# Optimization experiments

Measured on AMD Instinct MI355X. Metric: run time of the kernel, lower is better.

The kernel has to match this reference:

```python
import jax, jax.numpy as jnp
import numpy as np

N_DIM = 128
M_SEQ = 2048
BATCH = 256


def setup_inputs() -> dict:
    key = jax.random.key(0)
    k1, k2, k3 = jax.random.split(key, 3)
    scale = 1.0 / np.sqrt(N_DIM)
    return {
        "x": jax.random.normal(k1, (BATCH, N_DIM, M_SEQ), dtype=jnp.float32),
        "W": jax.random.normal(k2, (N_DIM, 3 * N_DIM), dtype=jnp.float32) * scale,
        "U": jax.random.normal(k3, (N_DIM, 3 * N_DIM), dtype=jnp.float32) * scale,
        "b": jnp.zeros((3 * N_DIM,), dtype=jnp.float32),
    }


def reference(x, W, U, b):
    # x: [B, D, T] -> scan over T with a GRU cell, output [B, D, T]
    B, D, T = x.shape
    xs = jnp.transpose(x, (2, 0, 1))  # [T, B, D]

    def cell(h, xt):
        gx = xt @ W + b              # [B, 3D]
        gh = h @ U                   # [B, 3D]
        xz, xr, xn = jnp.split(gx, 3, axis=-1)
        hz, hr, hn = jnp.split(gh, 3, axis=-1)
        z = jax.nn.sigmoid(xz + hz)  # update gate
        r = jax.nn.sigmoid(xr + hr)  # reset gate
        n = jnp.tanh(xn + r * hn)    # candidate
        h_new = z * h + (1.0 - z) * n
        return h_new, h_new

    h0 = jnp.zeros((B, D), dtype=x.dtype)
    _, ys = jax.lax.scan(cell, h0, xs)   # ys: [T, B, D]
    return jnp.transpose(ys, (1, 2, 0))  # [B, D, T]
```

## Files before the change

kernel.cpp:

```cpp
#include <hip/hip_runtime.h>

typedef float f32x4 __attribute__((ext_vector_type(4)));
typedef short bf16x8 __attribute__((ext_vector_type(8)));

#define TT    2048
#define DDIM  128
#define G3    384
#define NBBLK 16
#define GXROW 6144
#define GX_BYTES ((size_t)NBBLK * TT * GXROW * 2)

__device__ __forceinline__ unsigned f2bf_u(float f) {
    unsigned u = __float_as_uint(f);
    return (u + 0x7FFFu + ((u >> 16) & 1u)) >> 16;
}
__device__ __forceinline__ float bf_lo(unsigned u) { return __uint_as_float(u << 16); }
__device__ __forceinline__ float bf_hi(unsigned u) { return __uint_as_float(u & 0xffff0000u); }
__device__ __forceinline__ float rcp_(float x) { return __builtin_amdgcn_rcpf(x); }
__device__ __forceinline__ float sigm_(float v) { return rcp_(1.0f + __expf(-v)); }
__device__ __forceinline__ float tanhf_(float v) { return 2.0f * rcp_(1.0f + __expf(-2.0f * v)) - 1.0f; }

__global__ __launch_bounds__(256) void gx_gemm(
    const float* __restrict__ x, const float* __restrict__ W,
    const float* __restrict__ bias, unsigned short* __restrict__ gx)
{
    const int bblk  = blockIdx.x;
    const int ttile = blockIdx.y;
    const int tid = threadIdx.x;
    const int w  = tid >> 6;
    const int l  = tid & 63;
    const int lc = l & 15;
    const int lk = l >> 4;

    __shared__ unsigned short xs[16 * 16 * DDIM];

    const int tiles[6] = {2*w, 2*w+1, 2*w+8, 2*w+9, 2*w+16, 2*w+17};

    bf16x8 wfrag[6][4];
    f32x4  binit[6];
    #pragma unroll
    for (int i6 = 0; i6 < 6; ++i6) {
        const int c = tiles[i6] * 16 + lc;
        const float bv = bias[c];
        binit[i6] = (f32x4){bv, bv, bv, bv};
        #pragma unroll
        for (int kt = 0; kt < 4; ++kt) {
            bf16x8 f;
            #pragma unroll
            for (int jj = 0; jj < 8; ++jj) {
                const int k = kt * 32 + lk * 8 + jj;
                f[jj] = (short)f2bf_u(W[k * G3 + c]);
            }
            wfrag[i6][kt] = f;
        }
    }

    int inoff[4];
    #pragma unroll
    for (int kt = 0; kt < 4; ++kt)
        inoff[kt] = (lc * 256 + kt * 64 + lk * 16) ^ ((lc & 7) << 4);

    const float* xb = x + (size_t)bblk * 16 * DDIM * TT;
    const int t0blk = ttile * 128;
    const int tq = tid & 3;
    const int pbase = tid >> 2;

    for (int chunk = 0; chunk < 8; ++chunk) {
        __syncthreads();
        const int t0 = t0blk + chunk * 16 + tq * 4;
        #pragma unroll 4
        for (int pp = 0; pp < 32; ++pp) {
            const int p = pbase + pp * 64;
            const int r = p >> 7, d = p & 127;
            f32x4 v = *(const f32x4*)(xb + (size_t)p * TT + t0);
            const int base = ((r * 128 + d) * 2) ^ ((r & 7) << 4);
            #pragma unroll
            for (int j = 0; j < 4; ++j) {
                const int tloc = tq * 4 + j;
                xs[(tloc * 4096 + base) >> 1] = (unsigned short)f2bf_u(v[j]);
            }
        }
        __syncthreads();

        for (int t = 0; t < 16; ++t) {
            bf16x8 a[4];
            #pragma unroll
            for (int kt = 0; kt < 4; ++kt)
                a[kt] = *(const bf16x8*)((const char*)xs + t * 4096 + inoff[kt]);

            const int tglob = t0blk + chunk * 16 + t;
            #pragma unroll
            for (int i6 = 0; i6 < 6; ++i6) {
                f32x4 acc = binit[i6];
                #pragma unroll
                for (int kt = 0; kt < 4; ++kt)
                    acc = __builtin_amdgcn_mfma_f32_16x16x32_bf16(a[kt], wfrag[i6][kt], acc, 0, 0, 0);
                unsigned p0 = f2bf_u(acc[0]) | (f2bf_u(acc[1]) << 16);
                unsigned p1 = f2bf_u(acc[2]) | (f2bf_u(acc[3]) << 16);
                const int tt6 = tiles[i6];
                const int cb = tt6 & 7, g = tt6 >> 3;
                const size_t off = ((size_t)(bblk * TT + tglob) * 8 + cb) * 768
                                   + g * 256 + l * 4;
                *(uint2*)(gx + off) = make_uint2(p0, p1);
            }
        }
    }
}

__global__ __launch_bounds__(512, 2) void gru_rec(
    const unsigned short* __restrict__ gx, const float* __restrict__ U,
    float* __restrict__ out)
{
    const int bblk = blockIdx.x;
    const int tid  = threadIdx.x;
    const int w  = tid >> 6;
    const int l  = tid & 63;
    const int lc = l & 15, lk = l >> 4;
    const int c  = w * 16 + lc;

    bf16x8 uz[4], ur[4], un[4];
    #pragma unroll
    for (int kt = 0; kt < 4; ++kt) {
        bf16x8 fz, fr, fn;
        #pragma unroll
        for (int jj = 0; jj < 8; ++jj) {
            const int k = kt * 32 + lk * 8 + jj;
            fz[jj] = (short)f2bf_u(U[k * G3 + c]);
            fr[jj] = (short)f2bf_u(U[k * G3 + 128 + c]);
            fn[jj] = (short)f2bf_u(U[k * G3 + 256 + c]);
        }
        uz[kt] = fz; ur[kt] = fr; un[kt] = fn;
    }

    __shared__ unsigned short hsA[2 * 2048];
    __shared__ float hlds[16 * 16 * 128];
    #pragma unroll
    for (int i = tid; i < 4096; i += 512) hsA[i] = 0;

    int roff[4];
    #pragma unroll
    for (int kt = 0; kt < 4; ++kt)
        roff[kt] = (lc * 256 + kt * 64 + lk * 16) ^ ((lc & 7) << 4);

    int widx[4];
    int hwi[4];
    #pragma unroll
    for (int i = 0; i < 4; ++i) {
        const int r = lk * 4 + i;
        widx[i] = (r * 128 + c) ^ ((r & 7) << 3);
        hwi[i]  = r * 128 + (c ^ ((r & 7) << 2));
    }

    float hold[4] = {0.f, 0.f, 0.f, 0.f};

    const unsigned short* g0 = gx + ((size_t)bblk * TT * 8 + w) * 768 + l * 4;

    const int cfl = w * 16 + (l >> 2);
    const int qfl = l & 3;
    float* outfl = out + ((size_t)(bblk * 16) * DDIM + cfl) * TT + qfl * 4;

    uint2 rgz[4], rgr[4], rgn[4];
    #pragma unroll
    for (int d = 0; d < 4; ++d) {
        const unsigned short* gq = g0 + (size_t)d * GXROW;
        rgz[d] = *(const uint2*)(gq);
        rgr[d] = *(const uint2*)(gq + 256);
        rgn[d] = *(const uint2*)(gq + 512);
    }

    __syncthreads();

#define GATE(I, J)                                                            \
    {                                                                         \
        const float zz = sigm_(az[I]);                                        \
        const float rr = sigm_(ar[I]);                                        \
        const float uu = gn##I + rr * an[I];                                  \
        const float nn = tanhf_(uu);                                          \
        const float hn = nn + zz * (hold[I] - nn);                            \
        hold[I] = hn;                                                         \
        hlds[(J) * 2048 + hwi[I]] = hn;                                       \
        hsA[(((J) & 1) ^ 1) * 2048 + widx[I]] = (unsigned short)f2bf_u(hn);   \
    }

#define SUBSTEP(J, DOPF)                                                      \
    {                                                                         \
        uint2 pz = rgz[(J) & 3], pr = rgr[(J) & 3], pn = rgn[(J) & 3];        \
        f32x4 az, ar;                                                         \
        az[0] = bf_lo(pz.x); az[1] = bf_hi(pz.x);                             \
        az[2] = bf_lo(pz.y); az[3] = bf_hi(pz.y);                             \
        ar[0] = bf_lo(pr.x); ar[1] = bf_hi(pr.x);                             \
        ar[2] = bf_lo(pr.y); ar[3] = bf_hi(pr.y);                             \
        const float gn0 = bf_lo(pn.x), gn1 = bf_hi(pn.x);                     \
        const float gn2 = bf_lo(pn.y), gn3 = bf_hi(pn.y);                     \
        if (DOPF) {                                                           \
            const unsigned short* gq = gpt + (size_t)((J) + 4) * GXROW;       \
            rgz[(J) & 3] = *(const uint2*)(gq);                               \
            rgr[(J) & 3] = *(const uint2*)(gq + 256);                         \
            rgn[(J) & 3] = *(const uint2*)(gq + 512);                         \
        }                                                                     \
        const char* hb = (const char*)hsA + ((J) & 1) * 4096;                 \
        bf16x8 a0 = *(const bf16x8*)(hb + roff[0]);                           \
        bf16x8 a1 = *(const bf16x8*)(hb + roff[1]);                           \
        bf16x8 a2 = *(const bf16x8*)(hb + roff[2]);                           \
        bf16x8 a3 = *(const bf16x8*)(hb + roff[3]);                           \
        f32x4 an = (f32x4){0.f, 0.f, 0.f, 0.f};                               \
        az = __builtin_amdgcn_mfma_f32_16x16x32_bf16(a0, uz[0], az, 0, 0, 0); \
        ar = __builtin_amdgcn_mfma_f32_16x16x32_bf16(a0, ur[0], ar, 0, 0, 0); \
        an = __builtin_amdgcn_mfma_f32_16x16x32_bf16(a0, un[0], an, 0, 0, 0); \
        az = __builtin_amdgcn_mfma_f32_16x16x32_bf16(a1, uz[1], az, 0, 0, 0); \
        ar = __builtin_amdgcn_mfma_f32_16x16x32_bf16(a1, ur[1], ar, 0, 0, 0); \
        an = __builtin_amdgcn_mfma_f32_16x16x32_bf16(a1, un[1], an, 0, 0, 0); \
        az = __builtin_amdgcn_mfma_f32_16x16x32_bf16(a2, uz[2], az, 0, 0, 0); \
        ar = __builtin_amdgcn_mfma_f32_16x16x32_bf16(a2, ur[2], ar, 0, 0, 0); \
        an = __builtin_amdgcn_mfma_f32_16x16x32_bf16(a2, un[2], an, 0, 0, 0); \
        az = __builtin_amdgcn_mfma_f32_16x16x32_bf16(a3, uz[3], az, 0, 0, 0); \
        ar = __builtin_amdgcn_mfma_f32_16x16x32_bf16(a3, ur[3], ar, 0, 0, 0); \
        an = __builtin_amdgcn_mfma_f32_16x16x32_bf16(a3, un[3], an, 0, 0, 0); \
        GATE(0, J) GATE(1, J) GATE(2, J) GATE(3, J)                           \
        asm volatile("s_waitcnt lgkmcnt(0)" ::: "memory");                    \
        __builtin_amdgcn_s_barrier();                                         \
    }

#define FLUSH(T0)                                                             \
    _Pragma("unroll")                                                         \
    for (int r = 0; r < 16; ++r) {                                            \
        const int fr = r * 128 + (cfl ^ ((r & 7) << 2));                      \
        f32x4 v;                                                              \
        v[0] = hlds[(qfl * 4 + 0) * 2048 + fr];                               \
        v[1] = hlds[(qfl * 4 + 1) * 2048 + fr];                               \
        v[2] = hlds[(qfl * 4 + 2) * 2048 + fr];                               \
        v[3] = hlds[(qfl * 4 + 3) * 2048 + fr];                               \
        *(f32x4*)(outfl + (size_t)r * (DDIM * TT) + (T0)) = v;                \
    }

    for (int t = 0; t < TT - 16; t += 16) {
        const unsigned short* gpt = g0 + (size_t)t * GXROW;
        SUBSTEP(0, true)  SUBSTEP(1, true)  SUBSTEP(2, true)  SUBSTEP(3, true)
        SUBSTEP(4, true)  SUBSTEP(5, true)  SUBSTEP(6, true)  SUBSTEP(7, true)
        SUBSTEP(8, true)  SUBSTEP(9, true)  SUBSTEP(10, true) SUBSTEP(11, true)
        SUBSTEP(12, true) SUBSTEP(13, true) SUBSTEP(14, true) SUBSTEP(15, true)
        FLUSH(t)
    }
    {
        const int t = TT - 16;
        const unsigned short* gpt = g0 + (size_t)t * GXROW;
        SUBSTEP(0, true)  SUBSTEP(1, true)  SUBSTEP(2, true)  SUBSTEP(3, true)
        SUBSTEP(4, true)  SUBSTEP(5, true)  SUBSTEP(6, true)  SUBSTEP(7, true)
        SUBSTEP(8, true)  SUBSTEP(9, true)  SUBSTEP(10, true) SUBSTEP(11, true)
        SUBSTEP(12, false) SUBSTEP(13, false) SUBSTEP(14, false) SUBSTEP(15, false)
        FLUSH(t)
    }
#undef GATE
#undef SUBSTEP
#undef FLUSH
}

typedef float f32x2 __attribute__((ext_vector_type(2)));

__global__ __launch_bounds__(768) void gru_fused(
    const float* __restrict__ x, const float* __restrict__ W,
    const float* __restrict__ U, const float* __restrict__ b,
    float* __restrict__ out)
{
    const int bb  = blockIdx.x;
    const int tid = threadIdx.x;
    const int kh  = (tid >= G3) ? 1 : 0;
    const int c   = tid - kh * G3;
    const int kbase = kh * 64;

    f32x2 wcol[32], ucol[32];
    #pragma unroll
    for (int k2 = 0; k2 < 32; ++k2) {
        wcol[k2][0] = W[(size_t)(kbase + 2*k2 + 0) * G3 + c];
        wcol[k2][1] = W[(size_t)(kbase + 2*k2 + 1) * G3 + c];
        ucol[k2][0] = U[(size_t)(kbase + 2*k2 + 0) * G3 + c];
        ucol[k2][1] = U[(size_t)(kbase + 2*k2 + 1) * G3 + c];
    }
    const float bias = b[c];

    __shared__ float xs[2][DDIM];
    __shared__ float hs[DDIM];
    __shared__ float px[G3], ph[G3];
    __shared__ float rs[DDIM], ns[DDIM];

    if (tid < DDIM) { hs[tid] = 0.0f; xs[0][tid] = x[((size_t)bb * DDIM + tid) * TT]; }
    __syncthreads();

    const float* __restrict__ xrow = x   + (size_t)bb * DDIM * TT;
    float* __restrict__       orow = out + (size_t)bb * DDIM * TT;
    float zv = 0.0f;

    for (int t = 0; t < TT; ++t) {
        const float* xcur = xs[t & 1] + kbase;
        const float* hcur = hs + kbase;
        f32x2 axv = {0.f, 0.f}, ahv = {0.f, 0.f};
        #pragma unroll
        for (int k2 = 0; k2 < 32; ++k2) {
            f32x2 xv = *(const f32x2*)(xcur + 2*k2);
            f32x2 hv = *(const f32x2*)(hcur + 2*k2);
            axv += xv * wcol[k2];
            ahv += hv * ucol[k2];
        }
        float ax = axv[0] + axv[1];
        float ah = ahv[0] + ahv[1];
        if (kh) { px[c] = ax; ph[c] = ah; }
        if (t + 1 < TT && tid >= 128 && tid < 256) {
            const int k = tid - 128;
            xs[(t + 1) & 1][k] = xrow[(size_t)k * TT + (t + 1)];
        }
        __syncthreads();
        if (!kh) {
            ax += px[c]; ah += ph[c];
            if (c < DDIM)            zv = sigm_(ax + ah + bias);
            else if (c < 2*DDIM)     rs[c - DDIM] = sigm_(ax + ah + bias);
            else { px[c] = ax + bias; ph[c] = ah; }
        }
        __syncthreads();
        if (!kh && c >= 2*DDIM) {
            float r = rs[c - 2*DDIM];
            ns[c - 2*DDIM] = tanhf_(px[c] + r * ph[c]);
        }
        __syncthreads();
        if (tid < DDIM) {
            float n = ns[tid];
            float hnew = zv * hs[tid] + (1.0f - zv) * n;
            hs[tid] = hnew;
            orow[(size_t)tid * TT + t] = hnew;
        }
        __syncthreads();
    }
}

extern "C" void kernel_launch(void* const* d_in, const int* in_sizes, int n_in,
                              void* d_out, int out_size, void* d_ws, size_t ws_size,
                              hipStream_t stream) {
    const float* x = (const float*)d_in[0];
    const float* W = (const float*)d_in[1];
    const float* U = (const float*)d_in[2];
    const float* b = (const float*)d_in[3];
    float* out     = (float*)d_out;

    if (ws_size >= GX_BYTES) {
        unsigned short* gx = (unsigned short*)d_ws;
        hipLaunchKernelGGL(gx_gemm, dim3(16, 16), dim3(256), 0, stream, x, W, b, gx);
        hipLaunchKernelGGL(gru_rec, dim3(16), dim3(512), 0, stream, gx, U, out);
    } else {
        hipLaunchKernelGGL(gru_fused, dim3(256), dim3(768), 0, stream, x, W, U, b, out);
    }
}
```

Measured before the change: 1.812 ms.

## Split gate MFMA chains, use packed bf16 conversion, and reswizzle h staging LDS

Replaces the software float-to-bf16 rounding with the hardware v_cvt_pk_bf16_f32 instruction in both the input GEMM and the recurrence. Splits each gate's four-deep MFMA accumulation chain into two independent chains that are summed in the gate math, shortening the dependent latency on the serial per-timestep path. It also changes the LDS staging layout for the fp32 hidden history to a rotation-based swizzle with precomputed byte addresses, and moves the h-tile LDS reads ahead of the gx prefetch. The extra adds and a different bank pattern in the flush are the trade-offs.

```diff
diff --git a/kernel.cpp b/kernel.cpp
--- a/kernel.cpp
+++ b/kernel.cpp
@@ -19,6 +19,11 @@
 __device__ __forceinline__ float rcp_(float x) { return __builtin_amdgcn_rcpf(x); }
 __device__ __forceinline__ float sigm_(float v) { return rcp_(1.0f + __expf(-v)); }
 __device__ __forceinline__ float tanhf_(float v) { return 2.0f * rcp_(1.0f + __expf(-2.0f * v)) - 1.0f; }
+__device__ __forceinline__ unsigned cvt_pk_bf16(float lo, float hi) {
+    unsigned d;
+    asm("v_cvt_pk_bf16_f32 %0, %1, %2" : "=v"(d) : "v"(lo), "v"(hi));
+    return d;
+}
 
 __global__ __launch_bounds__(256) void gx_gemm(
     const float* __restrict__ x, const float* __restrict__ W,
@@ -73,12 +78,13 @@
             const int p = pbase + pp * 64;
             const int r = p >> 7, d = p & 127;
             f32x4 v = *(const f32x4*)(xb + (size_t)p * TT + t0);
-            const int base = ((r * 128 + d) * 2) ^ ((r & 7) << 4);
-            #pragma unroll
-            for (int j = 0; j < 4; ++j) {
-                const int tloc = tq * 4 + j;
-                xs[(tloc * 4096 + base) >> 1] = (unsigned short)f2bf_u(v[j]);
-            }
+            char* bp = (char*)xs + (tq * 4) * 4096 + (((r * 128 + d) * 2) ^ ((r & 7) << 4));
+            const unsigned pkA = cvt_pk_bf16(v[0], v[1]);
+            const unsigned pkB = cvt_pk_bf16(v[2], v[3]);
+            *(unsigned short*)(bp)         = (unsigned short)pkA;
+            *(unsigned short*)(bp + 4096)  = (unsigned short)(pkA >> 16);
+            *(unsigned short*)(bp + 8192)  = (unsigned short)pkB;
+            *(unsigned short*)(bp + 12288) = (unsigned short)(pkB >> 16);
         }
         __syncthreads();
 
@@ -95,8 +101,8 @@
                 #pragma unroll
                 for (int kt = 0; kt < 4; ++kt)
                     acc = __builtin_amdgcn_mfma_f32_16x16x32_bf16(a[kt], wfrag[i6][kt], acc, 0, 0, 0);
-                unsigned p0 = f2bf_u(acc[0]) | (f2bf_u(acc[1]) << 16);
-                unsigned p1 = f2bf_u(acc[2]) | (f2bf_u(acc[3]) << 16);
+                unsigned p0 = cvt_pk_bf16(acc[0], acc[1]);
+                unsigned p1 = cvt_pk_bf16(acc[2], acc[3]);
                 const int tt6 = tiles[i6];
                 const int cb = tt6 & 7, g = tt6 >> 3;
                 const size_t off = ((size_t)(bblk * TT + tglob) * 8 + cb) * 768
@@ -136,28 +142,40 @@
     __shared__ float hlds[16 * 16 * 128];
     #pragma unroll
     for (int i = tid; i < 4096; i += 512) hsA[i] = 0;
+    char* const hb_lds = (char*)hlds;
 
     int roff[4];
     #pragma unroll
     for (int kt = 0; kt < 4; ++kt)
         roff[kt] = (lc * 256 + kt * 64 + lk * 16) ^ ((lc & 7) << 4);
 
-    int widx[4];
-    int hwi[4];
+    unsigned widxB[4];
     #pragma unroll
     for (int i = 0; i < 4; ++i) {
         const int r = lk * 4 + i;
-        widx[i] = (r * 128 + c) ^ ((r & 7) << 3);
-        hwi[i]  = r * 128 + (c ^ ((r & 7) << 2));
-    }
-
-    float hold[4] = {0.f, 0.f, 0.f, 0.f};
-
-    const unsigned short* g0 = gx + ((size_t)bblk * TT * 8 + w) * 768 + l * 4;
+        widxB[i] = (unsigned)(((r * 128 + c) ^ ((r & 7) << 3)) * 2);
+    }
+
+    int hl_addr[4][4];
+    #pragma unroll
+    for (int s = 0; s < 4; ++s)
+        #pragma unroll
+        for (int i = 0; i < 4; ++i) {
+            const int r = lk * 4 + i;
+            hl_addr[s][i] = s * 32768 + (r * 128 + ((c + 8 * lk + 8 * s) & 127)) * 4;
+        }
 
     const int cfl = w * 16 + (l >> 2);
     const int qfl = l & 3;
-    float* outfl = out + ((size_t)(bblk * 16) * DDIM + cfl) * TT + qfl * 4;
+    int fl_base[4];
+    #pragma unroll
+    for (int g = 0; g < 4; ++g)
+        fl_base[g] = qfl * 32768 + ((cfl + 8 * g + 8 * qfl) & 127) * 4;
+
+    float hold[4] = {0.f, 0.f, 0.f, 0.f};
+
+    const unsigned short* g0 = gx + ((size_t)bblk * TT * 8 + w) * 768 + l * 4;
+    float* outb = out + (size_t)(bblk * 16) * DDIM * TT;
 
     uint2 rgz[4], rgr[4], rgn[4];
     #pragma unroll
@@ -172,51 +190,62 @@
 
 #define GATE(I, J)                                                            \
     {                                                                         \
-        const float zz = sigm_(az[I]);                                        \
-        const float rr = sigm_(ar[I]);                                        \
-        const float uu = gn##I + rr * an[I];                                  \
+        const float zz = sigm_(az_a[I] + az_b[I]);                            \
+        const float rr = sigm_(ar_a[I] + ar_b[I]);                            \
+        const float uu = gn##I + rr * (an_a[I] + an_b[I]);                    \
         const float nn = tanhf_(uu);                                          \
         const float hn = nn + zz * (hold[I] - nn);                            \
         hold[I] = hn;                                                         \
-        hlds[(J) * 2048 + hwi[I]] = hn;                                       \
-        hsA[(((J) & 1) ^ 1) * 2048 + widx[I]] = (unsigned short)f2bf_u(hn);   \
+        *(float*)(hb_lds + hl_addr[(J) >> 2][I] + ((J) & 3) * 8192) = hn;     \
+        hh[I] = hn;                                                           \
     }
 
 #define SUBSTEP(J, DOPF)                                                      \
     {                                                                         \
+        const char* hb = (const char*)hsA + ((J) & 1) * 4096;                 \
+        bf16x8 a0 = *(const bf16x8*)(hb + roff[0]);                           \
+        bf16x8 a1 = *(const bf16x8*)(hb + roff[1]);                           \
+        bf16x8 a2 = *(const bf16x8*)(hb + roff[2]);                           \
+        bf16x8 a3 = *(const bf16x8*)(hb + roff[3]);                           \
         uint2 pz = rgz[(J) & 3], pr = rgr[(J) & 3], pn = rgn[(J) & 3];        \
-        f32x4 az, ar;                                                         \
-        az[0] = bf_lo(pz.x); az[1] = bf_hi(pz.x);                             \
-        az[2] = bf_lo(pz.y); az[3] = bf_hi(pz.y);                             \
-        ar[0] = bf_lo(pr.x); ar[1] = bf_hi(pr.x);                             \
-        ar[2] = bf_lo(pr.y); ar[3] = bf_hi(pr.y);                             \
-        const float gn0 = bf_lo(pn.x), gn1 = bf_hi(pn.x);                     \
-        const float gn2 = bf_lo(pn.y), gn3 = bf_hi(pn.y);                     \
         if (DOPF) {                                                           \
             const unsigned short* gq = gpt + (size_t)((J) + 4) * GXROW;       \
             rgz[(J) & 3] = *(const uint2*)(gq);                               \
             rgr[(J) & 3] = *(const uint2*)(gq + 256);                         \
             rgn[(J) & 3] = *(const uint2*)(gq + 512);                         \
         }                                                                     \
-        const char* hb = (const char*)hsA + ((J) & 1) * 4096;                 \
-        bf16x8 a0 = *(const bf16x8*)(hb + roff[0]);                           \
-        bf16x8 a1 = *(const bf16x8*)(hb + roff[1]);                           \
-        bf16x8 a2 = *(const bf16x8*)(hb + roff[2]);                           \
-        bf16x8 a3 = *(const bf16x8*)(hb + roff[3]);                           \
-        f32x4 an = (f32x4){0.f, 0.f, 0.f, 0.f};                               \
-        az = __builtin_amdgcn_mfma_f32_16x16x32_bf16(a0, uz[0], az, 0, 0, 0); \
-        ar = __builtin_amdgcn_mfma_f32_16x16x32_bf16(a0, ur[0], ar, 0, 0, 0); \
-        an = __builtin_amdgcn_mfma_f32_16x16x32_bf16(a0, un[0], an, 0, 0, 0); \
-        az = __builtin_amdgcn_mfma_f32_16x16x32_bf16(a1, uz[1], az, 0, 0, 0); \
-        ar = __builtin_amdgcn_mfma_f32_16x16x32_bf16(a1, ur[1], ar, 0, 0, 0); \
-        an = __builtin_amdgcn_mfma_f32_16x16x32_bf16(a1, un[1], an, 0, 0, 0); \
-        az = __builtin_amdgcn_mfma_f32_16x16x32_bf16(a2, uz[2], az, 0, 0, 0); \
-        ar = __builtin_amdgcn_mfma_f32_16x16x32_bf16(a2, ur[2], ar, 0, 0, 0); \
-        an = __builtin_amdgcn_mfma_f32_16x16x32_bf16(a2, un[2], an, 0, 0, 0); \
-        az = __builtin_amdgcn_mfma_f32_16x16x32_bf16(a3, uz[3], az, 0, 0, 0); \
-        ar = __builtin_amdgcn_mfma_f32_16x16x32_bf16(a3, ur[3], ar, 0, 0, 0); \
-        an = __builtin_amdgcn_mfma_f32_16x16x32_bf16(a3, un[3], an, 0, 0, 0); \
+        f32x4 az_a, ar_a;                                                     \
+        az_a[0] = bf_lo(pz.x); az_a[1] = bf_hi(pz.x);                         \
+        az_a[2] = bf_lo(pz.y); az_a[3] = bf_hi(pz.y);                         \
+        ar_a[0] = bf_lo(pr.x); ar_a[1] = bf_hi(pr.x);                         \
+        ar_a[2] = bf_lo(pr.y); ar_a[3] = bf_hi(pr.y);                         \
+        const float gn0 = bf_lo(pn.x), gn1 = bf_hi(pn.x);                     \
+        const float gn2 = bf_lo(pn.y), gn3 = bf_hi(pn.y);                     \
+        f32x4 an_a = (f32x4){0.f, 0.f, 0.f, 0.f};                             \
+        f32x4 an_b = an_a, az_b = an_a, ar_b = an_a;                          \
+        an_a = __builtin_amdgcn_mfma_f32_16x16x32_bf16(a0, un[0], an_a, 0, 0, 0); \
+        an_b = __builtin_amdgcn_mfma_f32_16x16x32_bf16(a2, un[2], an_b, 0, 0, 0); \
+        az_a = __builtin_amdgcn_mfma_f32_16x16x32_bf16(a0, uz[0], az_a, 0, 0, 0); \
+        az_b = __builtin_amdgcn_mfma_f32_16x16x32_bf16(a2, uz[2], az_b, 0, 0, 0); \
+        ar_a = __builtin_amdgcn_mfma_f32_16x16x32_bf16(a0, ur[0], ar_a, 0, 0, 0); \
+        ar_b = __builtin_amdgcn_mfma_f32_16x16x32_bf16(a2, ur[2], ar_b, 0, 0, 0); \
+        an_a = __builtin_amdgcn_mfma_f32_16x16x32_bf16(a1, un[1], an_a, 0, 0, 0); \
+        an_b = __builtin_amdgcn_mfma_f32_16x16x32_bf16(a3, un[3], an_b, 0, 0, 0); \
+        az_a = __builtin_amdgcn_mfma_f32_16x16x32_bf16(a1, uz[1], az_a, 0, 0, 0); \
+        az_b = __builtin_amdgcn_mfma_f32_16x16x32_bf16(a3, uz[3], az_b, 0, 0, 0); \
+        ar_a = __builtin_amdgcn_mfma_f32_16x16x32_bf16(a1, ur[1], ar_a, 0, 0, 0); \
+        ar_b = __builtin_amdgcn_mfma_f32_16x16x32_bf16(a3, ur[3], ar_b, 0, 0, 0); \
+        float hh[4];                                                          \
         GATE(0, J) GATE(1, J) GATE(2, J) GATE(3, J)                           \
+        {                                                                     \
+            char* hwb = (char*)hsA + (((J) & 1) ^ 1) * 4096;                  \
+            const unsigned pk01 = cvt_pk_bf16(hh[0], hh[1]);                  \
+            const unsigned pk23 = cvt_pk_bf16(hh[2], hh[3]);                  \
+            *(unsigned short*)(hwb + widxB[0]) = (unsigned short)pk01;        \
+            *(unsigned short*)(hwb + widxB[1]) = (unsigned short)(pk01 >> 16);\
+            *(unsigned short*)(hwb + widxB[2]) = (unsigned short)pk23;        \
+            *(unsigned short*)(hwb + widxB[3]) = (unsigned short)(pk23 >> 16);\
+        }                                                                     \
         asm volatile("s_waitcnt lgkmcnt(0)" ::: "memory");                    \
         __builtin_amdgcn_s_barrier();                                         \
     }
@@ -224,13 +253,11 @@
 #define FLUSH(T0)                                                             \
     _Pragma("unroll")                                                         \
     for (int r = 0; r < 16; ++r) {                                            \
-        const int fr = r * 128 + (cfl ^ ((r & 7) << 2));                      \
         f32x4 v;                                                              \
-        v[0] = hlds[(qfl * 4 + 0) * 2048 + fr];                               \
-        v[1] = hlds[(qfl * 4 + 1) * 2048 + fr];                               \
-        v[2] = hlds[(qfl * 4 + 2) * 2048 + fr];                               \
-        v[3] = hlds[(qfl * 4 + 3) * 2048 + fr];                               \
-        *(f32x4*)(outfl + (size_t)r * (DDIM * TT) + (T0)) = v;                \
+        _Pragma("unroll")                                                     \
+        for (int k = 0; k < 4; ++k)                                           \
+            v[k] = *(const float*)(hb_lds + fl_base[r >> 2] + r * 512 + k * 8192); \
+        *(f32x4*)(outb + ((size_t)r * DDIM + cfl) * TT + (T0) + qfl * 4) = v; \
     }
 
     for (int t = 0; t < TT - 16; t += 16) {
```

New measurement: 1.797 ms. About the same (-0.8%).
